# Optimization experiments

Measured on AMD Instinct MI355X. Metric: run time of the kernel, lower is better.

## Reference

```python
import jax, jax.numpy as jnp
import numpy as np

N = 100000      # nodes
E = 3200000     # edges (avg degree 32)
F_IN = 512      # input features
H = 16          # hidden (module default)
C = 40          # classes


def _linear_params(key, fan_in, fan_out):
    # torch.nn.Linear default init: U(-1/sqrt(fan_in), 1/sqrt(fan_in))
    k1, k2 = jax.random.split(key)
    lim = 1.0 / np.sqrt(fan_in)
    W = jax.random.uniform(k1, (fan_in, fan_out), jnp.float32, -lim, lim)
    b = jax.random.uniform(k2, (fan_out,), jnp.float32, -lim, lim)
    return W, b


def setup_inputs() -> dict:
    key = jax.random.key(0)
    ks = jax.random.split(key, 8)
    x = jax.random.normal(ks[0], (N, F_IN), jnp.float32)
    edge_index = jax.random.randint(ks[1], (2, E), 0, N, dtype=jnp.int64)
    edge_weight = jax.random.uniform(ks[2], (E,), jnp.float32)
    W_first, b_first = _linear_params(ks[3], F_IN, H)
    W_conv1, b_conv1 = _linear_params(ks[4], H, H)
    W_conv2, b_conv2 = _linear_params(ks[5], H, H)
    W_out, b_out = _linear_params(ks[6], H, C)
    return {
        "x": x, "edge_index": edge_index, "edge_weight": edge_weight,
        "W_first": W_first, "b_first": b_first,
        "W_conv1": W_conv1, "b_conv1": b_conv1,
        "W_conv2": W_conv2, "b_conv2": b_conv2,
        "W_out": W_out, "b_out": b_out,
    }


def _gcn_conv(x, W, b, row, col, ew):
    # PyG GCNConv: h = x @ W; out_i = sum_{(j->i)} norm_e * h_j + b
    # norm_e = deg^-1/2[row] * w_e * deg^-1/2[col], deg from target (col) index,
    # with self-loops (weight 1) already appended to row/col/ew.
    n = x.shape[0]
    deg = jax.ops.segment_sum(ew, col, num_segments=n)
    dinv = jnp.where(deg > 0, jax.lax.rsqrt(deg), 0.0)
    norm = dinv[row] * ew * dinv[col]
    h = x @ W
    out = jax.ops.segment_sum(h[row] * norm[:, None], col, num_segments=n)
    return out + b


def reference(x, edge_index, edge_weight, W_first, b_first,
              W_conv1, b_conv1, W_conv2, b_conv2, W_out, b_out):
    n = x.shape[0]
    # add self-loops once (shared by all conv layers)
    loop = jnp.arange(n, dtype=edge_index.dtype)
    row = jnp.concatenate([edge_index[0], loop])
    col = jnp.concatenate([edge_index[1], loop])
    ew = jnp.concatenate([edge_weight, jnp.ones((n,), edge_weight.dtype)])

    h = jax.nn.relu(x @ W_first + b_first)
    # dropout: eval mode -> identity
    h = jax.nn.relu(_gcn_conv(h, W_conv1, b_conv1, row, col, ew))
    h = jax.nn.relu(_gcn_conv(h, W_conv2, b_conv2, row, col, ew))
    # dropout: eval mode -> identity
    logits = h @ W_out + b_out
    return jax.nn.log_softmax(logits, axis=-1)
```

## Files before the change

kernel.cpp:

```cpp
#include <hip/hip_runtime.h>
#include <hip/hip_bf16.h>
#include <math.h>

#define F_IN 512
#define H 16
#define BSH 7
#define BNODES (1 << BSH)
#define SSH 12
#define EPT 64
#define CAP 5376
#define SEG 4096
#define SL 33


__global__ __launch_bounds__(256) void hist_kernel(const int* __restrict__ col,
                                                   int* __restrict__ bcnt, int E, int NBUCK) {
    extern __shared__ int hs[];
    const int t = threadIdx.x;
    for (int i = t; i < NBUCK; i += 256) hs[i] = 0;
    __syncthreads();
    long long e0 = (long long)blockIdx.x * (256 * EPT) + t;
#pragma unroll 4
    for (int k = 0; k < EPT; ++k) {
        long long e = e0 + (long long)k * 256;
        if (e < E) atomicAdd(&hs[col[e] >> BSH], 1);
    }
    __syncthreads();
    for (int i = t; i < NBUCK; i += 256) {
        int h = hs[i];
        if (h > 0) atomicAdd(&bcnt[i], h);
    }
}

__global__ void bscan_kernel(const int* __restrict__ bcnt, int* __restrict__ bbase,
                             int* __restrict__ sbase, int* __restrict__ rowptr,
                             int NBUCK, int nsup, int E, int N) {
    __shared__ int sm[1024];
    int t = threadIdx.x;
    int v = (t < NBUCK) ? bcnt[t] : 0;
    sm[t] = v;
    __syncthreads();
    for (int o = 1; o < 1024; o <<= 1) {
        int u = (t >= o) ? sm[t - o] : 0;
        __syncthreads();
        sm[t] += u;
        __syncthreads();
    }
    if (t < NBUCK) bbase[t] = sm[t] - v;
    if (t == 0) { bbase[NBUCK] = E; rowptr[N] = E; }
    __syncthreads();
    if (t < nsup) {
        int bk = t << (SSH - BSH);
        sbase[t] = (bk < NBUCK) ? (sm[bk] - bcnt[bk]) : E;
    }
    if (t == nsup) sbase[nsup] = E;
}


__global__ __launch_bounds__(256) void scat1_kernel(const int* __restrict__ row,
                                                    const int* __restrict__ col,
                                                    const float* __restrict__ ew,
                                                    const int* __restrict__ sbase,
                                                    int* __restrict__ sfill,
                                                    int2* __restrict__ ptmp, int E, int nsup) {
    __shared__ int2 stg[SEG];
    __shared__ unsigned char sup[SEG];
    __shared__ int cnt[32], base[32];
    const int t = threadIdx.x;
    const int e0 = blockIdx.x * SEG;
    int m = E - e0; if (m > SEG) m = SEG;
    if (t < 32) cnt[t] = 0;
    __syncthreads();
    for (int i = t; i < m; i += 256) {
        int e = e0 + i;
        int c = col[e];
        int s = c >> SSH;
        sup[i] = (unsigned char)s;
        atomicAdd(&cnt[s], 1);
        stg[i] = make_int2(row[e] | ((c & ((1 << SSH) - 1)) << 17), __float_as_int(ew[e]));
    }
    __syncthreads();
    if (t < nsup) {
        int h = cnt[t];
        base[t] = h ? atomicAdd(&sfill[t], h) : 0;
        cnt[t] = 0;
    }
    __syncthreads();
    for (int i = t; i < m; i += 256) {
        int s = sup[i];
        int rk = atomicAdd(&cnt[s], 1);
        ptmp[sbase[s] + base[s] + rk] = stg[i];
    }
}


__global__ __launch_bounds__(256) void scat2_kernel(const int* __restrict__ sbase,
                                                    const int* __restrict__ bbase,
                                                    int* __restrict__ ffill,
                                                    const int2* __restrict__ ptmp,
                                                    int2* __restrict__ packed, int NBUCK) {
    __shared__ int2 stg[SEG];
    __shared__ int cnt[32], base[32];
    const int t = threadIdx.x;
    const int s  = blockIdx.x / SL;
    const int sl = blockIdx.x % SL;
    const int ss = sbase[s];
    const int len = sbase[s + 1] - ss;
    const int lo = ss + (int)((long long)len * sl / SL);
    const int hi = ss + (int)((long long)len * (sl + 1) / SL);
    int m = hi - lo; if (m > SEG) m = SEG;
    if (t < 32) cnt[t] = 0;
    __syncthreads();
    for (int i = t; i < m; i += 256) {
        int2 p = ptmp[lo + i];
        stg[i] = p;
        int bk5 = ((unsigned)p.x >> (17 + BSH)) & 31;
        atomicAdd(&cnt[bk5], 1);
    }
    __syncthreads();
    if (t < 32) {
        int bk = (s << 5) + t;
        int h = cnt[t];
        base[t] = (h && bk < NBUCK) ? atomicAdd(&ffill[bk], h) : 0;
        cnt[t] = 0;
    }
    __syncthreads();
    for (int i = t; i < m; i += 256) {
        int2 p = stg[i];
        int bk5 = ((unsigned)p.x >> (17 + BSH)) & 31;
        int rk = atomicAdd(&cnt[bk5], 1);
        int bk = (s << 5) + bk5;
        packed[bbase[bk] + base[bk5] + rk] = make_int2(p.x & 0xFFFFFF, p.y);
    }
}

__global__ __launch_bounds__(256) void pass2_kernel(const int* __restrict__ bbase,
                                                    int2* __restrict__ packed,
                                                    int* __restrict__ rowptr,
                                                    float* __restrict__ dinv, int N) {
    __shared__ int2  edg[CAP];
    __shared__ int   ncnt[BNODES], nsc[BNODES], nfill[BNODES];
    __shared__ float dsum[BNODES];
    const int t = threadIdx.x;
    const int b = blockIdx.x;
    const int s = bbase[b];
    int cnt = bbase[b + 1] - s;
    if (cnt > CAP) cnt = CAP;

    for (int i = t; i < cnt; i += 256) edg[i] = packed[s + i];
    if (t < BNODES) { ncnt[t] = 0; nfill[t] = 0; dsum[t] = 0.f; }
    __syncthreads();

    for (int i = t; i < cnt; i += 256) {
        int lc = (edg[i].x >> 17) & (BNODES - 1);
        atomicAdd(&ncnt[lc], 1);
        atomicAdd(&dsum[lc], __int_as_float(edg[i].y));
    }
    __syncthreads();
    if (t < BNODES) nsc[t] = ncnt[t];
    __syncthreads();
    for (int o = 1; o < BNODES; o <<= 1) {
        int v = (t < BNODES && t >= o) ? nsc[t - o] : 0;
        __syncthreads();
        if (t < BNODES) nsc[t] += v;
        __syncthreads();
    }
    if (t < BNODES) {
        int n = b * BNODES + t;
        if (n < N) {
            rowptr[n] = s + nsc[t] - ncnt[t];
            dinv[n]   = rsqrtf(1.0f + dsum[t]);
        }
    }
    __syncthreads();
    for (int i = t; i < cnt; i += 256) {
        int lc = (edg[i].x >> 17) & (BNODES - 1);
        int rk = atomicAdd(&nfill[lc], 1);
        packed[s + nsc[lc] - ncnt[lc] + rk] = make_int2(edg[i].x & 0x1FFFF, edg[i].y);
    }
}


#define L1_ROWS 8
#define XS_CH 36
#define XS_ROW (16 * XS_CH)

__global__ __launch_bounds__(256) void l1_kernel(const float* __restrict__ x,
                                                 const float* __restrict__ W,
                                                 const float* __restrict__ b,
                                                 float* __restrict__ h0, int N) {
    __shared__ float xs[L1_ROWS][XS_ROW];
    __shared__ float part[L1_ROWS][256];
    const int t  = threadIdx.x;
    const int o  = t & 15;
    const int fg = t >> 4;

    float Wreg[32];
#pragma unroll
    for (int j = 0; j < 32; ++j) Wreg[j] = W[(fg * 32 + j) * H + o];
    const float bias = b[o];

    const int nbatch = (N + L1_ROWS - 1) / L1_ROWS;
    for (int batch = blockIdx.x; batch < nbatch; batch += gridDim.x) {
        const int row0 = batch * L1_ROWS;
#pragma unroll
        for (int bq = 0; bq < 4; ++bq) {
            int L  = bq * 256 + t;
            int rl = L >> 7;
            int f4 = L & 127;
            int r  = row0 + rl;
            float4 v = make_float4(0.f, 0.f, 0.f, 0.f);
            if (r < N) v = *(const float4*)&x[(size_t)r * F_IN + f4 * 4];
            int fgs = f4 >> 3, j4 = f4 & 7;
            *(float4*)&xs[rl][fgs * XS_CH + j4 * 4] = v;
        }
        __syncthreads();

        float acc[L1_ROWS];
#pragma unroll
        for (int r = 0; r < L1_ROWS; ++r) acc[r] = 0.f;
#pragma unroll
        for (int j4 = 0; j4 < 8; ++j4) {
#pragma unroll
            for (int r = 0; r < L1_ROWS; ++r) {
                float4 xv = *(const float4*)&xs[r][fg * XS_CH + j4 * 4];
                acc[r] = fmaf(xv.x, Wreg[j4 * 4 + 0], acc[r]);
                acc[r] = fmaf(xv.y, Wreg[j4 * 4 + 1], acc[r]);
                acc[r] = fmaf(xv.z, Wreg[j4 * 4 + 2], acc[r]);
                acc[r] = fmaf(xv.w, Wreg[j4 * 4 + 3], acc[r]);
            }
        }
#pragma unroll
        for (int r = 0; r < L1_ROWS; ++r) part[r][fg * 16 + o] = acc[r];
        __syncthreads();

        if (t < 128) {
            int r = t >> 4, oo = t & 15;
            float s = 0.f;
#pragma unroll
            for (int g = 0; g < 16; ++g) s += part[r][g * 16 + oo];
            s = fmaxf(s + bias, 0.f);
            int rr = row0 + r;
            if (rr < N) h0[(size_t)rr * H + oo] = s;
        }
        __syncthreads();
    }
}


__global__ __launch_bounds__(256) void mm16_kernel(const float* __restrict__ hin,
                                                   const float* __restrict__ W,
                                                   const float* __restrict__ dinv,
                                                   float* __restrict__ hWs, int N) {
    __shared__ float Wl[H * H];
    if (threadIdx.x < H * H) Wl[threadIdx.x] = W[threadIdx.x];
    __syncthreads();
    int n = blockIdx.x * 256 + threadIdx.x;
    if (n >= N) return;
    float hv[H];
#pragma unroll
    for (int k4 = 0; k4 < 4; ++k4) {
        float4 v = *(const float4*)&hin[(size_t)n * H + k4 * 4];
        hv[k4 * 4 + 0] = v.x; hv[k4 * 4 + 1] = v.y;
        hv[k4 * 4 + 2] = v.z; hv[k4 * 4 + 3] = v.w;
    }
    float acc[H];
#pragma unroll
    for (int c = 0; c < H; ++c) acc[c] = 0.f;
#pragma unroll
    for (int k = 0; k < H; ++k) {
#pragma unroll
        for (int c = 0; c < H; ++c) acc[c] = fmaf(hv[k], Wl[k * H + c], acc[c]);
    }
    float di = dinv[n];
#pragma unroll
    for (int c4 = 0; c4 < 4; ++c4) {
        float4 a = make_float4(di * acc[c4 * 4], di * acc[c4 * 4 + 1],
                               di * acc[c4 * 4 + 2], di * acc[c4 * 4 + 3]);
        *(float4*)&hWs[(size_t)n * H + c4 * 4] = a;
    }
}


__global__ __launch_bounds__(256) void gather_kernel(const int* __restrict__ rowptr,
                                                     const int2* __restrict__ packed,
                                                     const float* __restrict__ hWs,
                                                     const float* __restrict__ dinv,
                                                     const float* __restrict__ b,
                                                     float* __restrict__ out, int N) {
    int t = blockIdx.x * 256 + threadIdx.x;
    int n = t >> 4, f = t & 15;
    if (n >= N) return;
    int s = rowptr[n], e = rowptr[n + 1];
    float acc = hWs[(size_t)n * H + f];
    int i = s;
    for (; i + 2 <= e; i += 2) {
        int2 p0 = packed[i], p1 = packed[i + 1];
        float h0 = hWs[(size_t)p0.x * H + f];
        float h1 = hWs[(size_t)p1.x * H + f];
        acc = fmaf(__int_as_float(p0.y), h0, acc);
        acc = fmaf(__int_as_float(p1.y), h1, acc);
    }
    if (i < e) {
        int2 p = packed[i];
        acc = fmaf(__int_as_float(p.y), hWs[(size_t)p.x * H + f], acc);
    }
    out[(size_t)n * H + f] = fmaxf(fmaf(dinv[n], acc, b[f]), 0.f);
}


__global__ __launch_bounds__(256) void out_kernel(const float* __restrict__ h,
                                                  const float* __restrict__ W,
                                                  const float* __restrict__ b,
                                                  float* __restrict__ out, int N, int C) {
    extern __shared__ float sm[];
    float* Wl = sm;
    float* bl = sm + H * C;
    for (int i = threadIdx.x; i < H * C; i += 256) Wl[i] = W[i];
    if (threadIdx.x < C) bl[threadIdx.x] = b[threadIdx.x];
    __syncthreads();
    int n = blockIdx.x * 256 + threadIdx.x;
    if (n >= N) return;
    float hv[H];
#pragma unroll
    for (int k4 = 0; k4 < 4; ++k4) {
        float4 v = *(const float4*)&h[(size_t)n * H + k4 * 4];
        hv[k4 * 4 + 0] = v.x; hv[k4 * 4 + 1] = v.y;
        hv[k4 * 4 + 2] = v.z; hv[k4 * 4 + 3] = v.w;
    }
    float acc[40];
    for (int c = 0; c < C; ++c) acc[c] = bl[c];
    for (int k = 0; k < H; ++k) {
        float xk = hv[k];
        for (int c = 0; c < C; ++c) acc[c] = fmaf(xk, Wl[k * C + c], acc[c]);
    }
    float m = -1e30f;
    for (int c = 0; c < C; ++c) m = fmaxf(m, acc[c]);
    float s = 0.f;
    for (int c = 0; c < C; ++c) s += __expf(acc[c] - m);
    float lse = m + __logf(s);
    for (int c = 0; c < C; ++c) acc[c] -= lse;
    for (int c4 = 0; c4 < C / 4; ++c4) {
        float4 v = make_float4(acc[c4 * 4], acc[c4 * 4 + 1], acc[c4 * 4 + 2], acc[c4 * 4 + 3]);
        *(float4*)&out[(size_t)n * C + c4 * 4] = v;
    }
}


extern "C" void kernel_launch(void* const* d_in, const int* in_sizes, int n_in,
                              void* d_out, int out_size, void* d_ws, size_t ws_size,
                              hipStream_t stream) {
    const float* x       = (const float*)d_in[0];
    const int*   ei      = (const int*)d_in[1];
    const float* ew      = (const float*)d_in[2];
    const float* W_first = (const float*)d_in[3];
    const float* b_first = (const float*)d_in[4];
    const float* W_c1    = (const float*)d_in[5];
    const float* b_c1    = (const float*)d_in[6];
    const float* W_c2    = (const float*)d_in[7];
    const float* b_c2    = (const float*)d_in[8];
    const float* W_o     = (const float*)d_in[9];
    const float* b_o     = (const float*)d_in[10];

    const int N = in_sizes[0] / F_IN;
    const int E = in_sizes[2];
    const int C = in_sizes[10];
    const int NBUCK = (N + BNODES - 1) >> BSH;
    const int NSUP  = ((N - 1) >> SSH) + 1;
    const int HB    = (E + 256 * EPT - 1) / (256 * EPT);
    const int SB    = (E + SEG - 1) / SEG;

    const int* row = ei;
    const int* col = ei + E;

    char* wsb = (char*)d_ws;
    int*   bcnt   = (int*)wsb;                  wsb += (size_t)NBUCK * 4;
    int*   sfill  = (int*)wsb;                  wsb += (size_t)32 * 4;
    int*   ffill  = (int*)wsb;                  wsb += (size_t)NBUCK * 4;
    int*   bbase  = (int*)wsb;                  wsb += (size_t)(NBUCK + 1) * 4;
    int*   sbase  = (int*)wsb;                  wsb += (size_t)(NSUP + 1) * 4;
    int*   rowptr = (int*)wsb;                  wsb += (size_t)(N + 1) * 4;
    float* dinv   = (float*)wsb;                wsb += (size_t)N * 4;
    int2*  packed = (int2*)wsb;                 wsb += (size_t)E * 8;
    int2*  ptmp   = (int2*)wsb;                 wsb += (size_t)E * 8;
    float* bufA   = (float*)ptmp;
    float* bufB   = (float*)d_out;

    hipMemsetAsync(bcnt, 0, (size_t)(NBUCK * 2 + 32) * 4, stream);

    hist_kernel<<<HB, 256, NBUCK * 4, stream>>>(col, bcnt, E, NBUCK);
    bscan_kernel<<<1, 1024, 0, stream>>>(bcnt, bbase, sbase, rowptr, NBUCK, NSUP, E, N);
    scat1_kernel<<<SB, 256, 0, stream>>>(row, col, ew, sbase, sfill, ptmp, E, NSUP);
    scat2_kernel<<<NSUP * SL, 256, 0, stream>>>(sbase, bbase, ffill, ptmp, packed, NBUCK);
    pass2_kernel<<<NBUCK, 256, 0, stream>>>(bbase, packed, rowptr, dinv, N);

    l1_kernel<<<1024, 256, 0, stream>>>(x, W_first, b_first, bufA, N);

    mm16_kernel<<<(N + 255) / 256, 256, 0, stream>>>(bufA, W_c1, dinv, bufB, N);
    gather_kernel<<<(N * 16 + 255) / 256, 256, 0, stream>>>(rowptr, packed, bufB, dinv, b_c1, bufA, N);

    mm16_kernel<<<(N + 255) / 256, 256, 0, stream>>>(bufA, W_c2, dinv, bufB, N);
    gather_kernel<<<(N * 16 + 255) / 256, 256, 0, stream>>>(rowptr, packed, bufB, dinv, b_c2, bufA, N);

    size_t smem = (size_t)(H * C + C) * sizeof(float);
    out_kernel<<<(N + 255) / 256, 256, smem, stream>>>(bufA, W_o, b_o, (float*)d_out, N, C);
}
```

Measured before the change: 687.3 us.

## Store hW in fp16 for gathers and retile first linear layer

The intermediate hW*dinv buffer read by the edge gather is now stored as fp16, which halves the bytes fetched per random neighbor access in both conv layers. Accumulation stays in fp32. Separately, the 512->16 first layer is retiled so each thread computes two output columns over 16 inputs, with 32 feature groups and a wider partial-sum reduction. Half precision adds rounding error to the aggregated features, which could matter against the reference tolerance.

```diff
diff --git a/kernel.cpp b/kernel.cpp
--- a/kernel.cpp
+++ b/kernel.cpp
@@ -1,5 +1,6 @@
 #include <hip/hip_runtime.h>
 #include <hip/hip_bf16.h>
+#include <hip/hip_fp16.h>
 #include <math.h>
 
 #define F_IN 512
@@ -182,23 +183,24 @@
 
 
 #define L1_ROWS 8
-#define XS_CH 36
-#define XS_ROW (16 * XS_CH)
+#define XS_CH 20
 
 __global__ __launch_bounds__(256) void l1_kernel(const float* __restrict__ x,
                                                  const float* __restrict__ W,
                                                  const float* __restrict__ b,
                                                  float* __restrict__ h0, int N) {
-    __shared__ float xs[L1_ROWS][XS_ROW];
-    __shared__ float part[L1_ROWS][256];
+    __shared__ float  xs[L1_ROWS][32 * XS_CH];
+    __shared__ float2 part[L1_ROWS][256];
     const int t  = threadIdx.x;
-    const int o  = t & 15;
-    const int fg = t >> 4;
-
-    float Wreg[32];
-#pragma unroll
-    for (int j = 0; j < 32; ++j) Wreg[j] = W[(fg * 32 + j) * H + o];
-    const float bias = b[o];
+    const int o  = t & 7;
+    const int fg = t >> 3;
+
+    float w0[16], w1[16];
+#pragma unroll
+    for (int j = 0; j < 16; ++j) {
+        w0[j] = W[(fg * 16 + j) * H + o];
+        w1[j] = W[(fg * 16 + j) * H + o + 8];
+    }
 
     const int nbatch = (N + L1_ROWS - 1) / L1_ROWS;
     for (int batch = blockIdx.x; batch < nbatch; batch += gridDim.x) {
@@ -211,35 +213,43 @@
             int r  = row0 + rl;
             float4 v = make_float4(0.f, 0.f, 0.f, 0.f);
             if (r < N) v = *(const float4*)&x[(size_t)r * F_IN + f4 * 4];
-            int fgs = f4 >> 3, j4 = f4 & 7;
-            *(float4*)&xs[rl][fgs * XS_CH + j4 * 4] = v;
+            int c = f4 >> 2, j4 = f4 & 3;
+            *(float4*)&xs[rl][c * XS_CH + j4 * 4] = v;
         }
         __syncthreads();
 
-        float acc[L1_ROWS];
-#pragma unroll
-        for (int r = 0; r < L1_ROWS; ++r) acc[r] = 0.f;
-#pragma unroll
-        for (int j4 = 0; j4 < 8; ++j4) {
+        float acc0[L1_ROWS], acc1[L1_ROWS];
+#pragma unroll
+        for (int r = 0; r < L1_ROWS; ++r) { acc0[r] = 0.f; acc1[r] = 0.f; }
+#pragma unroll
+        for (int j4 = 0; j4 < 4; ++j4) {
 #pragma unroll
             for (int r = 0; r < L1_ROWS; ++r) {
                 float4 xv = *(const float4*)&xs[r][fg * XS_CH + j4 * 4];
-                acc[r] = fmaf(xv.x, Wreg[j4 * 4 + 0], acc[r]);
-                acc[r] = fmaf(xv.y, Wreg[j4 * 4 + 1], acc[r]);
-                acc[r] = fmaf(xv.z, Wreg[j4 * 4 + 2], acc[r]);
-                acc[r] = fmaf(xv.w, Wreg[j4 * 4 + 3], acc[r]);
+                acc0[r] = fmaf(xv.x, w0[j4 * 4 + 0], acc0[r]);
+                acc0[r] = fmaf(xv.y, w0[j4 * 4 + 1], acc0[r]);
+                acc0[r] = fmaf(xv.z, w0[j4 * 4 + 2], acc0[r]);
+                acc0[r] = fmaf(xv.w, w0[j4 * 4 + 3], acc0[r]);
+                acc1[r] = fmaf(xv.x, w1[j4 * 4 + 0], acc1[r]);
+                acc1[r] = fmaf(xv.y, w1[j4 * 4 + 1], acc1[r]);
+                acc1[r] = fmaf(xv.z, w1[j4 * 4 + 2], acc1[r]);
+                acc1[r] = fmaf(xv.w, w1[j4 * 4 + 3], acc1[r]);
             }
         }
 #pragma unroll
-        for (int r = 0; r < L1_ROWS; ++r) part[r][fg * 16 + o] = acc[r];
+        for (int r = 0; r < L1_ROWS; ++r) part[r][fg * 8 + o] = make_float2(acc0[r], acc1[r]);
         __syncthreads();
 
         if (t < 128) {
             int r = t >> 4, oo = t & 15;
+            int o8 = oo & 7;
             float s = 0.f;
 #pragma unroll
-            for (int g = 0; g < 16; ++g) s += part[r][g * 16 + oo];
-            s = fmaxf(s + bias, 0.f);
+            for (int g = 0; g < 32; ++g) {
+                float2 p = part[r][g * 8 + o8];
+                s += (oo < 8) ? p.x : p.y;
+            }
+            s = fmaxf(s + b[oo], 0.f);
             int rr = row0 + r;
             if (rr < N) h0[(size_t)rr * H + oo] = s;
         }
@@ -251,7 +261,7 @@
 __global__ __launch_bounds__(256) void mm16_kernel(const float* __restrict__ hin,
                                                    const float* __restrict__ W,
                                                    const float* __restrict__ dinv,
-                                                   float* __restrict__ hWs, int N) {
+                                                   __half* __restrict__ hWs, int N) {
     __shared__ float Wl[H * H];
     if (threadIdx.x < H * H) Wl[threadIdx.x] = W[threadIdx.x];
     __syncthreads();
@@ -273,18 +283,18 @@
         for (int c = 0; c < H; ++c) acc[c] = fmaf(hv[k], Wl[k * H + c], acc[c]);
     }
     float di = dinv[n];
-#pragma unroll
-    for (int c4 = 0; c4 < 4; ++c4) {
-        float4 a = make_float4(di * acc[c4 * 4], di * acc[c4 * 4 + 1],
-                               di * acc[c4 * 4 + 2], di * acc[c4 * 4 + 3]);
-        *(float4*)&hWs[(size_t)n * H + c4 * 4] = a;
-    }
+    __half2 hp[8];
+#pragma unroll
+    for (int i = 0; i < 8; ++i)
+        hp[i] = __half2(__float2half(di * acc[2 * i]), __float2half(di * acc[2 * i + 1]));
+    *(uint4*)&hWs[(size_t)n * H]     = *(uint4*)&hp[0];
+    *(uint4*)&hWs[(size_t)n * H + 8] = *(uint4*)&hp[4];
 }
 
 
 __global__ __launch_bounds__(256) void gather_kernel(const int* __restrict__ rowptr,
                                                      const int2* __restrict__ packed,
-                                                     const float* __restrict__ hWs,
+                                                     const __half* __restrict__ hWs,
                                                      const float* __restrict__ dinv,
                                                      const float* __restrict__ b,
                                                      float* __restrict__ out, int N) {
@@ -292,18 +302,18 @@
     int n = t >> 4, f = t & 15;
     if (n >= N) return;
     int s = rowptr[n], e = rowptr[n + 1];
-    float acc = hWs[(size_t)n * H + f];
+    float acc = __half2float(hWs[(size_t)n * H + f]);
     int i = s;
     for (; i + 2 <= e; i += 2) {
         int2 p0 = packed[i], p1 = packed[i + 1];
-        float h0 = hWs[(size_t)p0.x * H + f];
-        float h1 = hWs[(size_t)p1.x * H + f];
+        float h0 = __half2float(hWs[(size_t)p0.x * H + f]);
+        float h1 = __half2float(hWs[(size_t)p1.x * H + f]);
         acc = fmaf(__int_as_float(p0.y), h0, acc);
         acc = fmaf(__int_as_float(p1.y), h1, acc);
     }
     if (i < e) {
         int2 p = packed[i];
-        acc = fmaf(__int_as_float(p.y), hWs[(size_t)p.x * H + f], acc);
+        acc = fmaf(__int_as_float(p.y), __half2float(hWs[(size_t)p.x * H + f]), acc);
     }
     out[(size_t)n * H + f] = fmaxf(fmaf(dinv[n], acc, b[f]), 0.f);
 }
@@ -383,8 +393,8 @@
     float* dinv   = (float*)wsb;                wsb += (size_t)N * 4;
     int2*  packed = (int2*)wsb;                 wsb += (size_t)E * 8;
     int2*  ptmp   = (int2*)wsb;                 wsb += (size_t)E * 8;
-    float* bufA   = (float*)ptmp;
-    float* bufB   = (float*)d_out;
+    float*  bufA  = (float*)ptmp;
+    __half* bufB  = (__half*)d_out;
 
     hipMemsetAsync(bcnt, 0, (size_t)(NBUCK * 2 + 32) * 4, stream);
 
```

New measurement: 696.3 us. No clear change (+1.3%).
